# Performance work log

Measured on AMD Instinct MI355X. Metric: run time of the kernel, lower is better.

The kernel has to match this reference:

```python
import jax, jax.numpy as jnp
import numpy as np

ALPHA = 0.2       # LeakyReLU negative slope
MASK_FILL = 1e-15 # value placed at non-edges before softmax (as in the original)
OUT_DIM = 64


def setup_inputs() -> dict:
    key = jax.random.key(0)
    k1, k2, k3, k4 = jax.random.split(key, 4)
    N, IN_DIM, D = 8192, 256, OUT_DIM
    h = jax.random.normal(k1, (N, IN_DIM), dtype=jnp.float32)
    # dense 0/1 adjacency (float, used only via A > 0)
    A = jax.random.randint(k2, (N, N), 0, 2).astype(jnp.float32)
    W = jax.random.normal(k3, (IN_DIM, D), dtype=jnp.float32) * (1.0 / np.sqrt(IN_DIM))
    a = jax.random.normal(k4, (2 * D,), dtype=jnp.float32) * (1.0 / np.sqrt(2 * D))
    return {"h": h, "A": A, "W": W, "a": a}


def reference(h, A, W, a):
    D = OUT_DIM
    Wh = h @ W                                   # [N, D]
    # attn([Wh_i || Wh_j]) == Wh_i . a[:D] + Wh_j . a[D:]  -- fused, avoids [N,N,2D]
    s_src = Wh @ a[:D]                           # [N]
    s_dst = Wh @ a[D:]                           # [N]
    e = jax.nn.leaky_relu(s_src[:, None] + s_dst[None, :], negative_slope=ALPHA)  # [N, N]
    attention = jnp.where(A > 0, e, MASK_FILL)
    attention = jax.nn.softmax(attention, axis=1)
    h_prime = attention @ Wh                     # [N, D]
    return jax.nn.elu(h_prime)                   # concat=True branch
```

## Files before the change

kernel.cpp:

```cpp
#include <hip/hip_runtime.h>
#include <hip/hip_bf16.h>

#define GAT_N 8192
#define GAT_K 256
#define GAT_D 64
#define GAT_ALPHA 0.2f
#define GAT_FILL 1e-15f

typedef float f32x4 __attribute__((ext_vector_type(4)));
typedef short bf16x8 __attribute__((ext_vector_type(8)));

static __device__ __forceinline__ unsigned f2bf_u(float x) {
  unsigned u = __float_as_uint(x);
  u += 0x7FFFu + ((u >> 16) & 1u);
  return u >> 16;
}

static __device__ __forceinline__ float rfl(float x) {
  return __uint_as_float(__builtin_amdgcn_readfirstlane(__float_as_uint(x)));
}

__global__ __launch_bounds__(256) void k_prep(const float* __restrict__ h,
                                              const float* __restrict__ W,
                                              const float* __restrict__ av,
                                              float* __restrict__ s_src,
                                              float* __restrict__ s_dst,
                                              short* __restrict__ WhT_f,
                                              float* __restrict__ bmax) {
  __shared__ short T[4][64][8];
  __shared__ float wmLds[4];
  const int tid = threadIdx.x;
  const int wv = tid >> 6, lane = tid & 63;
  const int r0 = blockIdx.x * 32 + wv * 8;

  float acc[8], acc2[8];
#pragma unroll
  for (int r = 0; r < 8; ++r) { acc[r] = 0.f; acc2[r] = 0.f; }

  for (int kc = 0; kc < GAT_K; kc += 32) {
    float Wreg[32];
#pragma unroll
    for (int e = 0; e < 32; ++e) Wreg[e] = W[(size_t)(kc + e) * GAT_D + lane];
#pragma unroll
    for (int r = 0; r < 8; ++r) {
      const f32x4* h4 = (const f32x4*)(h + (size_t)(r0 + r) * GAT_K + kc);
#pragma unroll
      for (int q = 0; q < 8; ++q) {
        f32x4 hv = h4[q];
        acc[r] += hv[0] * Wreg[4 * q + 0];
        acc2[r] += hv[1] * Wreg[4 * q + 1];
        acc[r] += hv[2] * Wreg[4 * q + 2];
        acc2[r] += hv[3] * Wreg[4 * q + 3];
      }
    }
  }

  const float a_s = av[lane];
  const float a_d = av[64 + lane];
  float wmax = -3.0e38f;
#pragma unroll
  for (int r = 0; r < 8; ++r) {
    const float accf = acc[r] + acc2[r];
    T[wv][lane][r] = (short)f2bf_u(accf);
    float vs = accf * a_s, vd = accf * a_d;
#pragma unroll
    for (int off = 32; off > 0; off >>= 1) {
      vs += __shfl_xor(vs, off);
      vd += __shfl_xor(vd, off);
    }
    if (lane == 0) { s_src[r0 + r] = vs; s_dst[r0 + r] = vd; }
    wmax = fmaxf(wmax, vd);
  }
  bf16x8 vt = *(const bf16x8*)&T[wv][lane][0];
  {
    const int c = r0 >> 9, f = (r0 & 511) >> 5, kgr = (r0 & 31) >> 3;
    short* dst = WhT_f + (size_t)c * 32768 + (size_t)(lane >> 4) * 8192 +
                 f * 512 + ((lane & 15) + 16 * kgr) * 8;
    *(bf16x8*)dst = vt;
  }

  if (lane == 0) wmLds[wv] = wmax;
  __syncthreads();
  if (tid == 0) {
    bmax[blockIdx.x] = fmaxf(fmaxf(wmLds[0], wmLds[1]), fmaxf(wmLds[2], wmLds[3]));
  }
}

__global__ __launch_bounds__(256, 6) void k_attn(
    const float* __restrict__ A,
    const float* __restrict__ s_src,
    const float* __restrict__ s_dst,
    const short* __restrict__ WhT_f,
    const float* __restrict__ bmax,
    float* __restrict__ o_part,
    float* __restrict__ l_part) {
  __shared__ char smem[16896];

  const int tid = threadIdx.x;
  const int wv = tid >> 6, lane = tid & 63;
  const int rsub = lane & 15, kg = lane >> 4;
  const int it = blockIdx.x >> 4, jc = blockIdx.x & 15;
  const int i0 = it * 16, j0 = jc * 512;

  float bm = fmaxf(fmaxf(bmax[lane], bmax[lane + 64]),
                   fmaxf(bmax[lane + 128], bmax[lane + 192]));
#pragma unroll
  for (int off = 32; off > 0; off >>= 1) bm = fmaxf(bm, __shfl_xor(bm, off));
  const float tmax = bm;

  const float* Arow = A + (size_t)(i0 + 4 * wv) * GAT_N + j0 + lane * 4;
  const f32x4 t0 = *(const f32x4*)(s_dst + j0 + lane * 4);
  const f32x4 t1 = *(const f32x4*)(s_dst + j0 + 256 + lane * 4);

  f32x4 E1a, E2a, E1b, E2b;
#pragma unroll
  for (int e = 0; e < 4; ++e) {
    E1a[e] = __expf(t0[e]);
    E2a[e] = __expf(GAT_ALPHA * t0[e]);
    E1b[e] = __expf(t1[e]);
    E2b[e] = __expf(GAT_ALPHA * t1[e]);
  }

#pragma unroll
  for (int r = 0; r < 4; ++r) {
    const int row = 4 * wv + r;
    f32x4 av0 = *(const f32x4*)(Arow + (size_t)r * GAT_N);
    f32x4 av1 = *(const f32x4*)(Arow + (size_t)r * GAT_N + 256);
    const float sc = rfl(s_src[i0 + row]);
    const float x0 = sc + tmax;
    const float m = fmaxf(fmaxf(x0, GAT_ALPHA * x0), GAT_FILL);
    const float F1 = rfl(__expf(sc - m));
    const float F2 = rfl(__expf(GAT_ALPHA * sc - m));
    const float ns = -sc;
    const float cc = rfl(__expf(GAT_FILL - m));

    float p[4];
#pragma unroll
    for (int e = 0; e < 4; ++e) {
      float psel = (t0[e] >= ns) ? E1a[e] * F1 : E2a[e] * F2;
      p[e] = (av0[e] > 0.f) ? psel : cc;
    }
    __hip_bfloat162 pa = __float22bfloat162_rn(float2{p[0], p[1]});
    __hip_bfloat162 pb = __float22bfloat162_rn(float2{p[2], p[3]});
    uint2 w;
    __builtin_memcpy(&w.x, &pa, 4);
    __builtin_memcpy(&w.y, &pb, 4);
    *(uint2*)(&smem[(row << 10) + ((lane << 3) ^ ((row & 7) << 4))]) = w;

#pragma unroll
    for (int e = 0; e < 4; ++e) {
      float psel = (t1[e] >= ns) ? E1b[e] * F1 : E2b[e] * F2;
      p[e] = (av1[e] > 0.f) ? psel : cc;
    }
    pa = __float22bfloat162_rn(float2{p[0], p[1]});
    pb = __float22bfloat162_rn(float2{p[2], p[3]});
    __builtin_memcpy(&w.x, &pa, 4);
    __builtin_memcpy(&w.y, &pb, 4);
    *(uint2*)(&smem[(row << 10) + ((512 + (lane << 3)) ^ ((row & 7) << 4))]) = w;
  }
  __syncthreads();

  bf16x8 ones;
#pragma unroll
  for (int e = 0; e < 8; ++e) ones[e] = (short)0x3F80;

  f32x4 acc0 = {0.f, 0.f, 0.f, 0.f};
  f32x4 acc1 = {0.f, 0.f, 0.f, 0.f};
  f32x4 acc2 = {0.f, 0.f, 0.f, 0.f};
  f32x4 acc3 = {0.f, 0.f, 0.f, 0.f};
  f32x4 accl = {0.f, 0.f, 0.f, 0.f};

  const short* Wb = WhT_f + (size_t)jc * 32768 + lane * 8;
#pragma unroll
  for (int q = 0; q < 4; ++q) {
    const int kq = wv * 4 + q;
    const int raddr = (rsub << 10) + (((kq << 6) | (kg << 4)) ^ ((rsub & 7) << 4));
    bf16x8 bP = *(const bf16x8*)(&smem[raddr]);
    bf16x8 a0 = *(const bf16x8*)(Wb + 0 * 8192 + kq * 512);
    bf16x8 a1 = *(const bf16x8*)(Wb + 1 * 8192 + kq * 512);
    bf16x8 a2 = *(const bf16x8*)(Wb + 2 * 8192 + kq * 512);
    bf16x8 a3 = *(const bf16x8*)(Wb + 3 * 8192 + kq * 512);
    acc0 = __builtin_amdgcn_mfma_f32_16x16x32_bf16(a0, bP, acc0, 0, 0, 0);
    acc1 = __builtin_amdgcn_mfma_f32_16x16x32_bf16(a1, bP, acc1, 0, 0, 0);
    acc2 = __builtin_amdgcn_mfma_f32_16x16x32_bf16(a2, bP, acc2, 0, 0, 0);
    acc3 = __builtin_amdgcn_mfma_f32_16x16x32_bf16(a3, bP, acc3, 0, 0, 0);
    accl = __builtin_amdgcn_mfma_f32_16x16x32_bf16(ones, bP, accl, 0, 0, 0);
  }
  __syncthreads();

  float* lds_o = (float*)smem;
  float* lds_l = (float*)(smem + 16640);
#pragma unroll
  for (int r = 0; r < 4; ++r) {
    const int d = kg * 4 + r;
    lds_o[wv * 1040 + rsub * 65 + 0 * 16 + d] = acc0[r];
    lds_o[wv * 1040 + rsub * 65 + 1 * 16 + d] = acc1[r];
    lds_o[wv * 1040 + rsub * 65 + 2 * 16 + d] = acc2[r];
    lds_o[wv * 1040 + rsub * 65 + 3 * 16 + d] = acc3[r];
  }
  if (kg == 0) lds_l[wv * 16 + rsub] = accl[0];
  __syncthreads();

  float* opb = o_part + ((size_t)jc * 512 + it) * 1024;
  for (int idx = tid; idx < 1024; idx += 256) {
    const int ii = idx >> 6, d = idx & 63;
    float o = lds_o[0 * 1040 + ii * 65 + d] + lds_o[1 * 1040 + ii * 65 + d] +
              lds_o[2 * 1040 + ii * 65 + d] + lds_o[3 * 1040 + ii * 65 + d];
    opb[idx] = o;
    if (d == 0) {
      l_part[jc * GAT_N + i0 + ii] = lds_l[0 * 16 + ii] + lds_l[1 * 16 + ii] +
                                     lds_l[2 * 16 + ii] + lds_l[3 * 16 + ii];
    }
  }
}

__global__ __launch_bounds__(256) void k_comb(const float* __restrict__ o_part,
                                              const float* __restrict__ l_part,
                                              float* __restrict__ out) {
  const int idx = blockIdx.x * 256 + threadIdx.x;
  const int gi = idx >> 4, d4 = (idx & 15) * 4;
  const int it = gi >> 4, ii = gi & 15;
  f32x4 o = {0.f, 0.f, 0.f, 0.f};
  float l = 0.f;
#pragma unroll
  for (int c = 0; c < 16; ++c) {
    o += *(const f32x4*)(o_part + ((size_t)c * 512 + it) * 1024 + ii * 64 + d4);
    l += l_part[c * GAT_N + gi];
  }
  f32x4 v;
#pragma unroll
  for (int e = 0; e < 4; ++e) {
    float val = o[e] / l;
    v[e] = (val > 0.f) ? val : (__expf(val) - 1.f);
  }
  *(f32x4*)(out + (size_t)gi * GAT_D + d4) = v;
}

extern "C" void kernel_launch(void* const* d_in, const int* in_sizes, int n_in,
                              void* d_out, int out_size, void* d_ws, size_t ws_size,
                              hipStream_t stream) {
  const float* h = (const float*)d_in[0];
  const float* A = (const float*)d_in[1];
  const float* W = (const float*)d_in[2];
  const float* a = (const float*)d_in[3];
  float* out = (float*)d_out;

  const size_t need = 2097152 + (size_t)16 * 512 * 1024 * 4;
  if (ws_size < need) return;
  float* bmax = (float*)d_ws;
  float* s_src = (float*)((char*)d_ws + 4096);
  float* s_dst = (float*)((char*)d_ws + 36864);
  short* WhT_f = (short*)((char*)d_ws + 69632);
  float* l_part = (float*)((char*)d_ws + 1572864);
  float* o_part = (float*)((char*)d_ws + 2097152);

  k_prep<<<dim3(256), dim3(256), 0, stream>>>(h, W, a, s_src, s_dst, WhT_f, bmax);
  k_attn<<<dim3(8192), dim3(256), 0, stream>>>(A, s_src, s_dst, WhT_f, bmax,
                                               o_part, l_part);
  k_comb<<<dim3(GAT_N * GAT_D / 1024), dim3(256), 0, stream>>>(o_part, l_part, out);
}
```

Measured before the change: 117.2 us.

## Enlarge attention tile to 64 rows and precompute per-row softmax constants

Each attention block now covers 64 rows with 512 threads instead of 16 rows with 256 threads. The WhT B-operand loads are reused across four MFMA row tiles, which cuts global reloads of Wh per row and removes per-block bmax reductions. Per-row softmax constants (exp factors, the negated source score and the fill constant) move to a new small kernel that writes them once. The cost is a much larger LDS footprint (66 KB), more accumulator registers and a two-phase LDS reduction, all of which may lower occupancy.

```diff
diff --git a/kernel.cpp b/kernel.cpp
--- a/kernel.cpp
+++ b/kernel.cpp
@@ -86,29 +86,44 @@
   }
 }
 
-__global__ __launch_bounds__(256, 6) void k_attn(
+__global__ __launch_bounds__(256) void k_scon(const float* __restrict__ s_src,
+                                              const float* __restrict__ bmax,
+                                              f32x4* __restrict__ scon) {
+  const int r = blockIdx.x * 256 + threadIdx.x;
+  const int lane = threadIdx.x & 63;
+  float bm = fmaxf(fmaxf(bmax[lane], bmax[lane + 64]),
+                   fmaxf(bmax[lane + 128], bmax[lane + 192]));
+#pragma unroll
+  for (int off = 32; off > 0; off >>= 1) bm = fmaxf(bm, __shfl_xor(bm, off));
+  const float tmax = bm;
+
+  const float sc = s_src[r];
+  const float x0 = sc + tmax;
+  const float m = fmaxf(fmaxf(x0, GAT_ALPHA * x0), GAT_FILL);
+  f32x4 s4;
+  s4[0] = __expf(sc - m);
+  s4[1] = __expf(GAT_ALPHA * sc - m);
+  s4[2] = -sc;
+  s4[3] = __expf(GAT_FILL - m);
+  scon[r] = s4;
+}
+
+__global__ __launch_bounds__(512, 4) void k_attn(
     const float* __restrict__ A,
-    const float* __restrict__ s_src,
     const float* __restrict__ s_dst,
+    const f32x4* __restrict__ scon,
     const short* __restrict__ WhT_f,
-    const float* __restrict__ bmax,
     float* __restrict__ o_part,
     float* __restrict__ l_part) {
-  __shared__ char smem[16896];
+  __shared__ char smem[67584];
 
   const int tid = threadIdx.x;
   const int wv = tid >> 6, lane = tid & 63;
   const int rsub = lane & 15, kg = lane >> 4;
   const int it = blockIdx.x >> 4, jc = blockIdx.x & 15;
-  const int i0 = it * 16, j0 = jc * 512;
-
-  float bm = fmaxf(fmaxf(bmax[lane], bmax[lane + 64]),
-                   fmaxf(bmax[lane + 128], bmax[lane + 192]));
-#pragma unroll
-  for (int off = 32; off > 0; off >>= 1) bm = fmaxf(bm, __shfl_xor(bm, off));
-  const float tmax = bm;
-
-  const float* Arow = A + (size_t)(i0 + 4 * wv) * GAT_N + j0 + lane * 4;
+  const int i0 = it * 64, j0 = jc * 512;
+
+  const float* Arow = A + (size_t)(i0 + 8 * wv) * GAT_N + j0 + lane * 4;
   const f32x4 t0 = *(const f32x4*)(s_dst + j0 + lane * 4);
   const f32x4 t1 = *(const f32x4*)(s_dst + j0 + 256 + lane * 4);
 
@@ -122,17 +137,13 @@
   }
 
 #pragma unroll
-  for (int r = 0; r < 4; ++r) {
-    const int row = 4 * wv + r;
+  for (int r = 0; r < 8; ++r) {
+    const int row = 8 * wv + r;
     f32x4 av0 = *(const f32x4*)(Arow + (size_t)r * GAT_N);
     f32x4 av1 = *(const f32x4*)(Arow + (size_t)r * GAT_N + 256);
-    const float sc = rfl(s_src[i0 + row]);
-    const float x0 = sc + tmax;
-    const float m = fmaxf(fmaxf(x0, GAT_ALPHA * x0), GAT_FILL);
-    const float F1 = rfl(__expf(sc - m));
-    const float F2 = rfl(__expf(GAT_ALPHA * sc - m));
-    const float ns = -sc;
-    const float cc = rfl(__expf(GAT_FILL - m));
+    const f32x4 s4 = scon[i0 + row];
+    const float F1 = rfl(s4[0]), F2 = rfl(s4[1]);
+    const float ns = rfl(s4[2]), cc = rfl(s4[3]);
 
     float p[4];
 #pragma unroll
@@ -164,52 +175,80 @@
 #pragma unroll
   for (int e = 0; e < 8; ++e) ones[e] = (short)0x3F80;
 
-  f32x4 acc0 = {0.f, 0.f, 0.f, 0.f};
-  f32x4 acc1 = {0.f, 0.f, 0.f, 0.f};
-  f32x4 acc2 = {0.f, 0.f, 0.f, 0.f};
-  f32x4 acc3 = {0.f, 0.f, 0.f, 0.f};
-  f32x4 accl = {0.f, 0.f, 0.f, 0.f};
+  f32x4 acc[4][4];
+  f32x4 accl[4];
+#pragma unroll
+  for (int dq = 0; dq < 4; ++dq)
+#pragma unroll
+    for (int n = 0; n < 4; ++n) acc[dq][n] = (f32x4){0.f, 0.f, 0.f, 0.f};
+#pragma unroll
+  for (int n = 0; n < 4; ++n) accl[n] = (f32x4){0.f, 0.f, 0.f, 0.f};
 
   const short* Wb = WhT_f + (size_t)jc * 32768 + lane * 8;
 #pragma unroll
-  for (int q = 0; q < 4; ++q) {
-    const int kq = wv * 4 + q;
-    const int raddr = (rsub << 10) + (((kq << 6) | (kg << 4)) ^ ((rsub & 7) << 4));
-    bf16x8 bP = *(const bf16x8*)(&smem[raddr]);
-    bf16x8 a0 = *(const bf16x8*)(Wb + 0 * 8192 + kq * 512);
-    bf16x8 a1 = *(const bf16x8*)(Wb + 1 * 8192 + kq * 512);
-    bf16x8 a2 = *(const bf16x8*)(Wb + 2 * 8192 + kq * 512);
-    bf16x8 a3 = *(const bf16x8*)(Wb + 3 * 8192 + kq * 512);
-    acc0 = __builtin_amdgcn_mfma_f32_16x16x32_bf16(a0, bP, acc0, 0, 0, 0);
-    acc1 = __builtin_amdgcn_mfma_f32_16x16x32_bf16(a1, bP, acc1, 0, 0, 0);
-    acc2 = __builtin_amdgcn_mfma_f32_16x16x32_bf16(a2, bP, acc2, 0, 0, 0);
-    acc3 = __builtin_amdgcn_mfma_f32_16x16x32_bf16(a3, bP, acc3, 0, 0, 0);
-    accl = __builtin_amdgcn_mfma_f32_16x16x32_bf16(ones, bP, accl, 0, 0, 0);
+  for (int q = 0; q < 2; ++q) {
+    const int kq = wv * 2 + q;
+    bf16x8 bP[4];
+#pragma unroll
+    for (int n = 0; n < 4; ++n) {
+      const int rr = n * 16 + rsub;
+      const int raddr = (rr << 10) + (((kq << 6) | (kg << 4)) ^ ((rr & 7) << 4));
+      bP[n] = *(const bf16x8*)(&smem[raddr]);
+    }
+#pragma unroll
+    for (int dq = 0; dq < 4; ++dq) {
+      bf16x8 a = *(const bf16x8*)(Wb + dq * 8192 + kq * 512);
+#pragma unroll
+      for (int n = 0; n < 4; ++n)
+        acc[dq][n] = __builtin_amdgcn_mfma_f32_16x16x32_bf16(a, bP[n], acc[dq][n], 0, 0, 0);
+    }
+#pragma unroll
+    for (int n = 0; n < 4; ++n)
+      accl[n] = __builtin_amdgcn_mfma_f32_16x16x32_bf16(ones, bP[n], accl[n], 0, 0, 0);
   }
   __syncthreads();
 
   float* lds_o = (float*)smem;
-  float* lds_l = (float*)(smem + 16640);
-#pragma unroll
-  for (int r = 0; r < 4; ++r) {
-    const int d = kg * 4 + r;
-    lds_o[wv * 1040 + rsub * 65 + 0 * 16 + d] = acc0[r];
-    lds_o[wv * 1040 + rsub * 65 + 1 * 16 + d] = acc1[r];
-    lds_o[wv * 1040 + rsub * 65 + 2 * 16 + d] = acc2[r];
-    lds_o[wv * 1040 + rsub * 65 + 3 * 16 + d] = acc3[r];
-  }
-  if (kg == 0) lds_l[wv * 16 + rsub] = accl[0];
-  __syncthreads();
-
-  float* opb = o_part + ((size_t)jc * 512 + it) * 1024;
-  for (int idx = tid; idx < 1024; idx += 256) {
+  float* lds_l = (float*)(smem + 66560);
+  if (wv < 4) {
+#pragma unroll
+    for (int dq = 0; dq < 4; ++dq)
+#pragma unroll
+      for (int n = 0; n < 4; ++n)
+#pragma unroll
+        for (int r = 0; r < 4; ++r)
+          lds_o[wv * 4160 + (n * 16 + rsub) * 65 + dq * 16 + kg * 4 + r] = acc[dq][n][r];
+    if (kg == 0) {
+#pragma unroll
+      for (int n = 0; n < 4; ++n) lds_l[wv * 64 + n * 16 + rsub] = accl[n][0];
+    }
+  }
+  __syncthreads();
+  if (wv >= 4) {
+    const int w2 = wv - 4;
+#pragma unroll
+    for (int dq = 0; dq < 4; ++dq)
+#pragma unroll
+      for (int n = 0; n < 4; ++n)
+#pragma unroll
+        for (int r = 0; r < 4; ++r)
+          lds_o[w2 * 4160 + (n * 16 + rsub) * 65 + dq * 16 + kg * 4 + r] += acc[dq][n][r];
+    if (kg == 0) {
+#pragma unroll
+      for (int n = 0; n < 4; ++n) lds_l[w2 * 64 + n * 16 + rsub] += accl[n][0];
+    }
+  }
+  __syncthreads();
+
+  float* opb = o_part + (size_t)jc * (GAT_N * 64) + (size_t)i0 * 64;
+  for (int idx = tid; idx < 64 * 64; idx += 512) {
     const int ii = idx >> 6, d = idx & 63;
-    float o = lds_o[0 * 1040 + ii * 65 + d] + lds_o[1 * 1040 + ii * 65 + d] +
-              lds_o[2 * 1040 + ii * 65 + d] + lds_o[3 * 1040 + ii * 65 + d];
+    float o = lds_o[0 * 4160 + ii * 65 + d] + lds_o[1 * 4160 + ii * 65 + d] +
+              lds_o[2 * 4160 + ii * 65 + d] + lds_o[3 * 4160 + ii * 65 + d];
     opb[idx] = o;
     if (d == 0) {
-      l_part[jc * GAT_N + i0 + ii] = lds_l[0 * 16 + ii] + lds_l[1 * 16 + ii] +
-                                     lds_l[2 * 16 + ii] + lds_l[3 * 16 + ii];
+      l_part[jc * GAT_N + i0 + ii] = lds_l[0 * 64 + ii] + lds_l[1 * 64 + ii] +
+                                     lds_l[2 * 64 + ii] + lds_l[3 * 64 + ii];
     }
   }
 }
@@ -219,12 +258,11 @@
                                               float* __restrict__ out) {
   const int idx = blockIdx.x * 256 + threadIdx.x;
   const int gi = idx >> 4, d4 = (idx & 15) * 4;
-  const int it = gi >> 4, ii = gi & 15;
   f32x4 o = {0.f, 0.f, 0.f, 0.f};
   float l = 0.f;
 #pragma unroll
   for (int c = 0; c < 16; ++c) {
-    o += *(const f32x4*)(o_part + ((size_t)c * 512 + it) * 1024 + ii * 64 + d4);
+    o += *(const f32x4*)(o_part + (size_t)c * (GAT_N * 64) + (size_t)gi * 64 + d4);
     l += l_part[c * GAT_N + gi];
   }
   f32x4 v;
@@ -245,7 +283,7 @@
   const float* a = (const float*)d_in[3];
   float* out = (float*)d_out;
 
-  const size_t need = 2097152 + (size_t)16 * 512 * 1024 * 4;
+  const size_t need = 35651584 + 131072;
   if (ws_size < need) return;
   float* bmax = (float*)d_ws;
   float* s_src = (float*)((char*)d_ws + 4096);
@@ -253,9 +291,11 @@
   short* WhT_f = (short*)((char*)d_ws + 69632);
   float* l_part = (float*)((char*)d_ws + 1572864);
   float* o_part = (float*)((char*)d_ws + 2097152);
+  f32x4* scon = (f32x4*)((char*)d_ws + 35651584);
 
   k_prep<<<dim3(256), dim3(256), 0, stream>>>(h, W, a, s_src, s_dst, WhT_f, bmax);
-  k_attn<<<dim3(8192), dim3(256), 0, stream>>>(A, s_src, s_dst, WhT_f, bmax,
-                                               o_part, l_part);
+  k_scon<<<dim3(GAT_N / 256), dim3(256), 0, stream>>>(s_src, bmax, scon);
+  k_attn<<<dim3(2048), dim3(512), 0, stream>>>(A, s_dst, scon, WhT_f, o_part,
+                                               l_part);
   k_comb<<<dim3(GAT_N * GAT_D / 1024), dim3(256), 0, stream>>>(o_part, l_part, out);
 }
```

Result: slower. 122.9 us (+4.9%).

## Precompute per-row softmax constants and hoist all global loads up front

Applied to the files above, without the earlier changes.

Adds a small kernel that computes the per-row max-derived constants (exp factors, negated score, fill value) once, so the attention kernel no longer reduces bmax and evaluates exps per block. The attention kernel now issues all eight A-row loads and the WhT operand loads before the LDS barrier, giving more memory-level parallelism. Occupancy hint drops from 6 to 4 blocks per CU to make room for the extra registers. This adds a kernel launch and a workspace buffer, and lower occupancy could hurt latency hiding.

```diff
diff --git a/kernel.cpp b/kernel.cpp
--- a/kernel.cpp
+++ b/kernel.cpp
@@ -86,12 +86,33 @@
   }
 }
 
-__global__ __launch_bounds__(256, 6) void k_attn(
+__global__ __launch_bounds__(256) void k_scon(const float* __restrict__ s_src,
+                                              const float* __restrict__ bmax,
+                                              f32x4* __restrict__ scon) {
+  const int r = blockIdx.x * 256 + threadIdx.x;
+  const int lane = threadIdx.x & 63;
+  float bm = fmaxf(fmaxf(bmax[lane], bmax[lane + 64]),
+                   fmaxf(bmax[lane + 128], bmax[lane + 192]));
+#pragma unroll
+  for (int off = 32; off > 0; off >>= 1) bm = fmaxf(bm, __shfl_xor(bm, off));
+  const float tmax = bm;
+
+  const float sc = s_src[r];
+  const float x0 = sc + tmax;
+  const float m = fmaxf(fmaxf(x0, GAT_ALPHA * x0), GAT_FILL);
+  f32x4 s4;
+  s4[0] = __expf(sc - m);
+  s4[1] = __expf(GAT_ALPHA * sc - m);
+  s4[2] = -sc;
+  s4[3] = __expf(GAT_FILL - m);
+  scon[r] = s4;
+}
+
+__global__ __launch_bounds__(256, 4) void k_attn(
     const float* __restrict__ A,
-    const float* __restrict__ s_src,
     const float* __restrict__ s_dst,
+    const f32x4* __restrict__ scon,
     const short* __restrict__ WhT_f,
-    const float* __restrict__ bmax,
     float* __restrict__ o_part,
     float* __restrict__ l_part) {
   __shared__ char smem[16896];
@@ -102,15 +123,22 @@
   const int it = blockIdx.x >> 4, jc = blockIdx.x & 15;
   const int i0 = it * 16, j0 = jc * 512;
 
-  float bm = fmaxf(fmaxf(bmax[lane], bmax[lane + 64]),
-                   fmaxf(bmax[lane + 128], bmax[lane + 192]));
-#pragma unroll
-  for (int off = 32; off > 0; off >>= 1) bm = fmaxf(bm, __shfl_xor(bm, off));
-  const float tmax = bm;
-
   const float* Arow = A + (size_t)(i0 + 4 * wv) * GAT_N + j0 + lane * 4;
+  f32x4 av0 = *(const f32x4*)(Arow + 0 * GAT_N);
+  f32x4 av1 = *(const f32x4*)(Arow + 0 * GAT_N + 256);
+  f32x4 av2 = *(const f32x4*)(Arow + 1 * GAT_N);
+  f32x4 av3 = *(const f32x4*)(Arow + 1 * GAT_N + 256);
+  f32x4 av4 = *(const f32x4*)(Arow + 2 * GAT_N);
+  f32x4 av5 = *(const f32x4*)(Arow + 2 * GAT_N + 256);
+  f32x4 av6 = *(const f32x4*)(Arow + 3 * GAT_N);
+  f32x4 av7 = *(const f32x4*)(Arow + 3 * GAT_N + 256);
+
   const f32x4 t0 = *(const f32x4*)(s_dst + j0 + lane * 4);
   const f32x4 t1 = *(const f32x4*)(s_dst + j0 + 256 + lane * 4);
+  const f32x4 sc0 = scon[i0 + 4 * wv + 0];
+  const f32x4 sc1 = scon[i0 + 4 * wv + 1];
+  const f32x4 sc2 = scon[i0 + 4 * wv + 2];
+  const f32x4 sc3 = scon[i0 + 4 * wv + 3];
 
   f32x4 E1a, E2a, E1b, E2b;
 #pragma unroll
@@ -121,24 +149,14 @@
     E2b[e] = __expf(GAT_ALPHA * t1[e]);
   }
 
-#pragma unroll
-  for (int r = 0; r < 4; ++r) {
-    const int row = 4 * wv + r;
-    f32x4 av0 = *(const f32x4*)(Arow + (size_t)r * GAT_N);
-    f32x4 av1 = *(const f32x4*)(Arow + (size_t)r * GAT_N + 256);
-    const float sc = rfl(s_src[i0 + row]);
-    const float x0 = sc + tmax;
-    const float m = fmaxf(fmaxf(x0, GAT_ALPHA * x0), GAT_FILL);
-    const float F1 = rfl(__expf(sc - m));
-    const float F2 = rfl(__expf(GAT_ALPHA * sc - m));
-    const float ns = -sc;
-    const float cc = rfl(__expf(GAT_FILL - m));
-
+  auto stage = [&](int row, const f32x4& avA, const f32x4& avB, const f32x4& s4) {
+    const float F1 = rfl(s4[0]), F2 = rfl(s4[1]);
+    const float ns = rfl(s4[2]), cc = rfl(s4[3]);
     float p[4];
 #pragma unroll
     for (int e = 0; e < 4; ++e) {
       float psel = (t0[e] >= ns) ? E1a[e] * F1 : E2a[e] * F2;
-      p[e] = (av0[e] > 0.f) ? psel : cc;
+      p[e] = (avA[e] > 0.f) ? psel : cc;
     }
     __hip_bfloat162 pa = __float22bfloat162_rn(float2{p[0], p[1]});
     __hip_bfloat162 pb = __float22bfloat162_rn(float2{p[2], p[3]});
@@ -150,14 +168,30 @@
 #pragma unroll
     for (int e = 0; e < 4; ++e) {
       float psel = (t1[e] >= ns) ? E1b[e] * F1 : E2b[e] * F2;
-      p[e] = (av1[e] > 0.f) ? psel : cc;
+      p[e] = (avB[e] > 0.f) ? psel : cc;
     }
     pa = __float22bfloat162_rn(float2{p[0], p[1]});
     pb = __float22bfloat162_rn(float2{p[2], p[3]});
     __builtin_memcpy(&w.x, &pa, 4);
     __builtin_memcpy(&w.y, &pb, 4);
     *(uint2*)(&smem[(row << 10) + ((512 + (lane << 3)) ^ ((row & 7) << 4))]) = w;
-  }
+  };
+
+  stage(4 * wv + 0, av0, av1, sc0);
+  stage(4 * wv + 1, av2, av3, sc1);
+  stage(4 * wv + 2, av4, av5, sc2);
+  stage(4 * wv + 3, av6, av7, sc3);
+
+  const short* Wb = WhT_f + (size_t)jc * 32768 + lane * 8;
+  bf16x8 wa[4][4];
+#pragma unroll
+  for (int q = 0; q < 4; ++q) {
+    const int kq = wv * 4 + q;
+#pragma unroll
+    for (int dq = 0; dq < 4; ++dq)
+      wa[q][dq] = *(const bf16x8*)(Wb + dq * 8192 + kq * 512);
+  }
+
   __syncthreads();
 
   bf16x8 ones;
@@ -170,20 +204,15 @@
   f32x4 acc3 = {0.f, 0.f, 0.f, 0.f};
   f32x4 accl = {0.f, 0.f, 0.f, 0.f};
 
-  const short* Wb = WhT_f + (size_t)jc * 32768 + lane * 8;
 #pragma unroll
   for (int q = 0; q < 4; ++q) {
     const int kq = wv * 4 + q;
     const int raddr = (rsub << 10) + (((kq << 6) | (kg << 4)) ^ ((rsub & 7) << 4));
     bf16x8 bP = *(const bf16x8*)(&smem[raddr]);
-    bf16x8 a0 = *(const bf16x8*)(Wb + 0 * 8192 + kq * 512);
-    bf16x8 a1 = *(const bf16x8*)(Wb + 1 * 8192 + kq * 512);
-    bf16x8 a2 = *(const bf16x8*)(Wb + 2 * 8192 + kq * 512);
-    bf16x8 a3 = *(const bf16x8*)(Wb + 3 * 8192 + kq * 512);
-    acc0 = __builtin_amdgcn_mfma_f32_16x16x32_bf16(a0, bP, acc0, 0, 0, 0);
-    acc1 = __builtin_amdgcn_mfma_f32_16x16x32_bf16(a1, bP, acc1, 0, 0, 0);
-    acc2 = __builtin_amdgcn_mfma_f32_16x16x32_bf16(a2, bP, acc2, 0, 0, 0);
-    acc3 = __builtin_amdgcn_mfma_f32_16x16x32_bf16(a3, bP, acc3, 0, 0, 0);
+    acc0 = __builtin_amdgcn_mfma_f32_16x16x32_bf16(wa[q][0], bP, acc0, 0, 0, 0);
+    acc1 = __builtin_amdgcn_mfma_f32_16x16x32_bf16(wa[q][1], bP, acc1, 0, 0, 0);
+    acc2 = __builtin_amdgcn_mfma_f32_16x16x32_bf16(wa[q][2], bP, acc2, 0, 0, 0);
+    acc3 = __builtin_amdgcn_mfma_f32_16x16x32_bf16(wa[q][3], bP, acc3, 0, 0, 0);
     accl = __builtin_amdgcn_mfma_f32_16x16x32_bf16(ones, bP, accl, 0, 0, 0);
   }
   __syncthreads();
@@ -245,7 +274,7 @@
   const float* a = (const float*)d_in[3];
   float* out = (float*)d_out;
 
-  const size_t need = 2097152 + (size_t)16 * 512 * 1024 * 4;
+  const size_t need = 35651584 + 131072;
   if (ws_size < need) return;
   float* bmax = (float*)d_ws;
   float* s_src = (float*)((char*)d_ws + 4096);
@@ -253,9 +282,11 @@
   short* WhT_f = (short*)((char*)d_ws + 69632);
   float* l_part = (float*)((char*)d_ws + 1572864);
   float* o_part = (float*)((char*)d_ws + 2097152);
+  f32x4* scon = (f32x4*)((char*)d_ws + 35651584);
 
   k_prep<<<dim3(256), dim3(256), 0, stream>>>(h, W, a, s_src, s_dst, WhT_f, bmax);
-  k_attn<<<dim3(8192), dim3(256), 0, stream>>>(A, s_src, s_dst, WhT_f, bmax,
-                                               o_part, l_part);
+  k_scon<<<dim3(GAT_N / 256), dim3(256), 0, stream>>>(s_src, bmax, scon);
+  k_attn<<<dim3(8192), dim3(256), 0, stream>>>(A, s_dst, scon, WhT_f, o_part,
+                                               l_part);
   k_comb<<<dim3(GAT_N * GAT_D / 1024), dim3(256), 0, stream>>>(o_part, l_part, out);
 }
```

Measured after the change: 119.9 us. 1.02x slower.
